# Performance work log

Measured on AMD Instinct MI355X. Metric: run time of the kernel, lower is better.

## Reference

```python
import jax, jax.numpy as jnp
import numpy as np

N_HEADS = 4


def setup_inputs() -> dict:
    key = jax.random.key(0)
    k1, k2, k3 = jax.random.split(key, 3)
    B, C, H, W = 16, 512, 32, 32
    x = jax.random.normal(k1, (B, C, H, W), dtype=jnp.float32)
    # Linear weights stored as (in, out) so y = x @ w + b
    w_proj = jax.random.normal(k2, (C, 3 * C), dtype=jnp.float32) * (C ** -0.5)
    b_proj = jnp.zeros((3 * C,), dtype=jnp.float32)
    w_out = jax.random.normal(k3, (C, C), dtype=jnp.float32) * (C ** -0.5)
    b_out = jnp.zeros((C,), dtype=jnp.float32)
    return {"x": x, "w_proj": w_proj, "b_proj": b_proj, "w_out": w_out, "b_out": b_out}


def reference(x, w_proj, b_proj, w_out, b_out):
    B, C, H, W = x.shape
    d_k = C // N_HEADS
    scale = d_k ** -0.5
    # NOTE: original module defines GroupNorm but never applies it in forward.
    xf = x.reshape(B, C, H * W).transpose(0, 2, 1)          # (B, N, C)
    qkv = xf @ w_proj + b_proj                                # (B, N, 3C)
    qkv = qkv.reshape(B, -1, N_HEADS, 3 * d_k)
    q, k, v = jnp.split(qkv, 3, axis=-1)                      # each (B, N, H, d_k)
    attn = jnp.einsum('bihd,bjhd->bijh', q, k) * scale        # (B, N, N, H)
    attn = jax.nn.softmax(attn, axis=2)                       # softmax over j
    res = jnp.einsum('bijh,bjhd->bihd', attn, v)              # (B, N, H, d_k)
    res = res.reshape(B, -1, N_HEADS * d_k)                   # (B, N, C)
    res = res @ w_out + b_out + xf                            # residual add
    return res.transpose(0, 2, 1).reshape(B, C, H, W)
```

## Files before the change

### kernel.cpp

```cpp
#include <hip/hip_runtime.h>

#define B_  16
#define C_  512
#define N_  1024
#define NH  4
#define DK  128
#define M3  1536

typedef unsigned short u16;
typedef unsigned int   u32;
typedef __attribute__((ext_vector_type(8))) short bfrag;
typedef __attribute__((ext_vector_type(4))) float f4;

#define MFMA(a, b, c) __builtin_amdgcn_mfma_f32_16x16x32_bf16(a, b, c, 0, 0, 0)

#define GL2LDS(gp, lp) __builtin_amdgcn_global_load_lds( \
    (__attribute__((address_space(1))) const unsigned int*)(const void*)(gp), \
    (__attribute__((address_space(3))) unsigned int*)(void*)(lp), 16, 0, 0)

__device__ __forceinline__ u16 f2bf(float f) {
    u32 u = __float_as_uint(f);
    return (u16)((u + 0x7FFFu + ((u >> 16) & 1u)) >> 16);
}
__device__ __forceinline__ float bf2f(u16 h) { return __uint_as_float(((u32)h) << 16); }

#define QSCL 0.12751741859316937f

__global__ __launch_bounds__(256) void conv_split_t(
    const float* __restrict__ src, u16* __restrict__ dhi, u16* __restrict__ dlo,
    int R, int Cc)
{
    __shared__ float Ts[64][65];
    const int tid = threadIdx.x;
    const int c0 = blockIdx.x * 64, r0 = blockIdx.y * 64;
    const size_t bofs = (size_t)blockIdx.z * R * Cc;

#pragma unroll
    for (int p = 0; p < 4; ++p) {
        int r = p * 16 + (tid >> 4);
        int c = (tid & 15) * 4;
        float4 v = *(const float4*)(src + bofs + (size_t)(r0 + r) * Cc + c0 + c);
        Ts[c + 0][r] = v.x; Ts[c + 1][r] = v.y; Ts[c + 2][r] = v.z; Ts[c + 3][r] = v.w;
    }
    __syncthreads();
#pragma unroll
    for (int p = 0; p < 4; ++p) {
        int cc = p * 16 + (tid >> 4);
        int rr = (tid & 15) * 4;
        float f0 = Ts[cc][rr + 0], f1 = Ts[cc][rr + 1];
        float f2 = Ts[cc][rr + 2], f3 = Ts[cc][rr + 3];
        u16 h0 = f2bf(f0), h1 = f2bf(f1), h2 = f2bf(f2), h3 = f2bf(f3);
        u16 l0 = f2bf(f0 - bf2f(h0)), l1 = f2bf(f1 - bf2f(h1));
        u16 l2 = f2bf(f2 - bf2f(h2)), l3 = f2bf(f3 - bf2f(h3));
        size_t o = bofs + (size_t)(c0 + cc) * R + r0 + rr;
        *(uint2*)(void*)(dhi + o) = make_uint2((u32)h0 | ((u32)h1 << 16), (u32)h2 | ((u32)h3 << 16));
        *(uint2*)(void*)(dlo + o) = make_uint2((u32)l0 | ((u32)l1 << 16), (u32)l2 | ((u32)l3 << 16));
    }
}

__global__ __launch_bounds__(256, 2) void qkv_mfma(
    const u16* __restrict__ xt_hi, const u16* __restrict__ xt_lo,
    const u16* __restrict__ wpT_hi, const u16* __restrict__ wpT_lo,
    const float* __restrict__ bp,
    u16* __restrict__ Qh, u16* __restrict__ Ql,
    u16* __restrict__ Kh, u16* __restrict__ Kl,
    u16* __restrict__ Vth, u16* __restrict__ Vtl)
{
    __shared__ __align__(16) u32 SMEM[16512];
    u16* AH = (u16*)SMEM;
    u16* AL = AH + 128 * 64;
    u16* BH = AL + 128 * 64;
    u16* BL = BH + 128 * 64;
    float* FB = (float*)SMEM;

    const int tid = threadIdx.x;
    const int l = tid & 63, w = tid >> 6;
    const int wr = w >> 1, wc = w & 1;
    const int lm = l & 15, kg = l >> 4;
    const int bx = blockIdx.x, by = blockIdx.y, b = blockIdx.z;
    const int m0 = bx * 128, n0 = by * 128;

    const u16* gsrc =
        (w == 0) ? xt_hi + ((size_t)b * N_ + n0) * C_ :
        (w == 1) ? xt_lo + ((size_t)b * N_ + n0) * C_ :
        (w == 2) ? wpT_hi + (size_t)m0 * C_ :
                   wpT_lo + (size_t)m0 * C_;
    u16* ldst = (w == 0) ? AH : (w == 1) ? AL : (w == 2) ? BH : BL;
    const int lane_off = (l >> 3) * C_ + (((l & 7) ^ (l >> 3)) << 3);

    f4 acc[4][4] = {};

    for (int it = 0; it < 8; ++it) {
        __syncthreads();
        const u16* g = gsrc + it * 64 + lane_off;
#pragma unroll
        for (int u = 0; u < 16; ++u)
            GL2LDS(g + (size_t)u * 8 * C_, ldst + u * 512);
        __syncthreads();

#pragma unroll
        for (int kk = 0; kk < 2; ++kk) {
            bfrag ah[4], al[4], bh[4], bl[4];
            const int s = ((kk * 4 + kg) ^ (lm & 7)) << 3;
#pragma unroll
            for (int f = 0; f < 4; ++f) {
                const int ar = wr * 64 + f * 16 + lm;
                const int br = wc * 64 + f * 16 + lm;
                ah[f] = *(const bfrag*)(AH + ar * 64 + s);
                al[f] = *(const bfrag*)(AL + ar * 64 + s);
                bh[f] = *(const bfrag*)(BH + br * 64 + s);
                bl[f] = *(const bfrag*)(BL + br * 64 + s);
            }
#pragma unroll
            for (int i = 0; i < 4; ++i)
#pragma unroll
                for (int j = 0; j < 4; ++j) {
                    acc[i][j] = MFMA(ah[i], bh[j], acc[i][j]);
                    acc[i][j] = MFMA(ah[i], bl[j], acc[i][j]);
                    acc[i][j] = MFMA(al[i], bh[j], acc[i][j]);
                }
        }
    }

    const int hh = bx / 3, t = bx - hh * 3;
    __syncthreads();
    {
        float bias_j[4];
#pragma unroll
        for (int j = 0; j < 4; ++j) bias_j[j] = bp[m0 + wc * 64 + j * 16 + lm];
#pragma unroll
        for (int j = 0; j < 4; ++j) {
            const int col = wc * 64 + j * 16 + lm;
#pragma unroll
            for (int i = 0; i < 4; ++i) {
#pragma unroll
                for (int r = 0; r < 4; ++r) {
                    const int tok = wr * 64 + i * 16 + kg * 4 + r;
                    float v = acc[i][j][r] + bias_j[j];
                    if (t == 0) v *= QSCL;
                    if (t == 2) FB[col * 129 + tok] = v;
                    else        FB[tok * 129 + col] = v;
                }
            }
        }
    }
    __syncthreads();
    {
        const int r2 = tid >> 1, h = tid & 1;
        const float* src = FB + r2 * 129 + h * 64;
        u16* dsth; u16* dstl; size_t o;
        if (t == 2) {
            dsth = Vth; dstl = Vtl;
            o = ((size_t)(b * NH + hh) * DK + r2) * N_ + n0 + h * 64;
        } else {
            dsth = (t == 0) ? Qh : Kh;
            dstl = (t == 0) ? Ql : Kl;
            o = ((size_t)(b * NH + hh) * N_ + n0 + r2) * DK + h * 64;
        }
#pragma unroll
        for (int c0 = 0; c0 < 64; c0 += 8) {
            u16 hb[8], lb[8];
#pragma unroll
            for (int c = 0; c < 8; ++c) {
                float v = src[c0 + c];
                hb[c] = f2bf(v);
                lb[c] = f2bf(v - bf2f(hb[c]));
            }
            *(uint4*)(void*)(dsth + o + c0) = make_uint4(
                (u32)hb[0] | ((u32)hb[1] << 16), (u32)hb[2] | ((u32)hb[3] << 16),
                (u32)hb[4] | ((u32)hb[5] << 16), (u32)hb[6] | ((u32)hb[7] << 16));
            *(uint4*)(void*)(dstl + o + c0) = make_uint4(
                (u32)lb[0] | ((u32)lb[1] << 16), (u32)lb[2] | ((u32)lb[3] << 16),
                (u32)lb[4] | ((u32)lb[5] << 16), (u32)lb[6] | ((u32)lb[7] << 16));
        }
    }
}

__global__ __launch_bounds__(256, 2) void attn_mfma(
    const u16* __restrict__ Qh_, const u16* __restrict__ Ql_,
    const u16* __restrict__ Kh_, const u16* __restrict__ Kl_,
    const u16* __restrict__ Vth_, const u16* __restrict__ Vtl_,
    u16* __restrict__ res_hi, u16* __restrict__ res_lo)
{
    __shared__ __align__(16) u16 KH[32 * 128], KL[32 * 128];
    __shared__ __align__(16) u16 VH[128 * 32], VL[128 * 32];
    __shared__ u16 Ph[4][2][16][40], Pl[4][2][16][40];

    const int tid = threadIdx.x;
    const int l = tid & 63, w = tid >> 6;
    const int lm = l & 15, kg = l >> 4;
    const int bh = blockIdx.x;
    const int qc = blockIdx.y;
    const int i0s = qc * 128 + w * 16 + lm;
    const size_t head = (size_t)bh * N_ * DK;

    bfrag qfh[2][4], qfl[2][4];
#pragma unroll
    for (int s = 0; s < 2; ++s) {
        const u16* qp  = Qh_ + head + (size_t)(i0s + s * 64) * DK + kg * 8;
        const u16* qp2 = Ql_ + head + (size_t)(i0s + s * 64) * DK + kg * 8;
#pragma unroll
        for (int kc = 0; kc < 4; ++kc) {
            qfh[s][kc] = *(const bfrag*)(qp + kc * 32);
            qfl[s][kc] = *(const bfrag*)(qp2 + kc * 32);
        }
    }

    f4 acc_o[2][8] = {};
    float m_r[2] = {-3.0e38f, -3.0e38f}, l_r[2] = {0.f, 0.f};

    for (int jt = 0; jt < 32; ++jt) {
        __syncthreads();
        if (w < 2) {
            const u16* sg = (w & 1) ? Kl_ : Kh_;
            u16* sd = (w & 1) ? KL : KH;
#pragma unroll
            for (int u = 0; u < 8; ++u) {
                const int rbase = u * 4;
                const int row = rbase + (l >> 4);
                GL2LDS(sg + head + (size_t)(jt * 32 + row) * DK + (((l & 15) ^ (row & 7)) << 3),
                       sd + rbase * 128);
            }
        } else {
            const u16* sg = (w & 1) ? Vtl_ : Vth_;
            u16* sd = (w & 1) ? VL : VH;
#pragma unroll
            for (int u = 0; u < 8; ++u) {
                const int rbase = u * 16;
                const int row = rbase + (l >> 2);
                GL2LDS(sg + (size_t)bh * DK * N_ + (size_t)row * N_ + jt * 32
                           + (((l & 3) ^ (row & 3)) << 3),
                       sd + rbase * 32);
            }
        }
        __syncthreads();

        f4 sacc[2][2] = {};
#pragma unroll
        for (int kc = 0; kc < 4; ++kc) {
#pragma unroll
            for (int jf = 0; jf < 2; ++jf) {
                const int row = jf * 16 + lm;
                const int sw = (((kc << 2) | kg) ^ (lm & 7)) << 3;
                bfrag kh = *(const bfrag*)(KH + row * 128 + sw);
                bfrag kl = *(const bfrag*)(KL + row * 128 + sw);
#pragma unroll
                for (int s = 0; s < 2; ++s) {
                    sacc[s][jf] = MFMA(kh, qfh[s][kc], sacc[s][jf]);
                    sacc[s][jf] = MFMA(kh, qfl[s][kc], sacc[s][jf]);
                    sacc[s][jf] = MFMA(kl, qfh[s][kc], sacc[s][jf]);
                }
            }
        }

        float mt[2], mn[2], alpha[2], rs[2];
#pragma unroll
        for (int s = 0; s < 2; ++s) {
            float a = fmaxf(fmaxf(sacc[s][0][0], sacc[s][0][1]),
                            fmaxf(sacc[s][0][2], sacc[s][0][3]));
            float bb = fmaxf(fmaxf(sacc[s][1][0], sacc[s][1][1]),
                             fmaxf(sacc[s][1][2], sacc[s][1][3]));
            mt[s] = fmaxf(a, bb);
        }
        mt[0] = fmaxf(mt[0], __shfl_xor(mt[0], 16));
        mt[1] = fmaxf(mt[1], __shfl_xor(mt[1], 16));
        mt[0] = fmaxf(mt[0], __shfl_xor(mt[0], 32));
        mt[1] = fmaxf(mt[1], __shfl_xor(mt[1], 32));
#pragma unroll
        for (int s = 0; s < 2; ++s) {
            mn[s] = fmaxf(m_r[s], mt[s]);
            alpha[s] = exp2f(m_r[s] - mn[s]);
            m_r[s] = mn[s];
            rs[s] = 0.f;
#pragma unroll
            for (int jf = 0; jf < 2; ++jf) {
                u16 hb[4], lb[4];
#pragma unroll
                for (int r = 0; r < 4; ++r) {
                    float pv = exp2f(sacc[s][jf][r] - mn[s]);
                    rs[s] += pv;
                    hb[r] = f2bf(pv);
                    lb[r] = f2bf(pv - bf2f(hb[r]));
                }
                *(uint2*)(void*)&Ph[w][s][lm][jf * 16 + kg * 4] =
                    make_uint2((u32)hb[0] | ((u32)hb[1] << 16), (u32)hb[2] | ((u32)hb[3] << 16));
                *(uint2*)(void*)&Pl[w][s][lm][jf * 16 + kg * 4] =
                    make_uint2((u32)lb[0] | ((u32)lb[1] << 16), (u32)lb[2] | ((u32)lb[3] << 16));
            }
        }
        rs[0] += __shfl_xor(rs[0], 16);
        rs[1] += __shfl_xor(rs[1], 16);
        rs[0] += __shfl_xor(rs[0], 32);
        rs[1] += __shfl_xor(rs[1], 32);
#pragma unroll
        for (int s = 0; s < 2; ++s) {
            l_r[s] = l_r[s] * alpha[s] + rs[s];
#pragma unroll
            for (int df = 0; df < 8; ++df)
#pragma unroll
                for (int r = 0; r < 4; ++r) acc_o[s][df][r] *= alpha[s];
        }

        bfrag pbh0 = *(const bfrag*)&Ph[w][0][lm][kg * 8];
        bfrag pbl0 = *(const bfrag*)&Pl[w][0][lm][kg * 8];
        bfrag pbh1 = *(const bfrag*)&Ph[w][1][lm][kg * 8];
        bfrag pbl1 = *(const bfrag*)&Pl[w][1][lm][kg * 8];
#pragma unroll
        for (int df = 0; df < 8; ++df) {
            const int row = df * 16 + lm;
            const int sw = (kg ^ (lm & 3)) << 3;
            bfrag vh = *(const bfrag*)(VH + row * 32 + sw);
            bfrag vl = *(const bfrag*)(VL + row * 32 + sw);
            acc_o[0][df] = MFMA(vh, pbh0, acc_o[0][df]);
            acc_o[0][df] = MFMA(vh, pbl0, acc_o[0][df]);
            acc_o[0][df] = MFMA(vl, pbh0, acc_o[0][df]);
            acc_o[1][df] = MFMA(vh, pbh1, acc_o[1][df]);
            acc_o[1][df] = MFMA(vh, pbl1, acc_o[1][df]);
            acc_o[1][df] = MFMA(vl, pbh1, acc_o[1][df]);
        }
    }

    const int b = bh >> 2, h = bh & 3;
#pragma unroll
    for (int s = 0; s < 2; ++s) {
        const float inv = 1.f / l_r[s];
        const size_t ro = ((size_t)b * N_ + i0s + s * 64) * C_ + h * DK;
#pragma unroll
        for (int df = 0; df < 8; ++df) {
            u16 hb[4], lb[4];
#pragma unroll
            for (int r = 0; r < 4; ++r) {
                float v = acc_o[s][df][r] * inv;
                hb[r] = f2bf(v);
                lb[r] = f2bf(v - bf2f(hb[r]));
            }
            const size_t o = ro + df * 16 + kg * 4;
            *(uint2*)(void*)(res_hi + o) = make_uint2((u32)hb[0] | ((u32)hb[1] << 16),
                                                      (u32)hb[2] | ((u32)hb[3] << 16));
            *(uint2*)(void*)(res_lo + o) = make_uint2((u32)lb[0] | ((u32)lb[1] << 16),
                                                      (u32)lb[2] | ((u32)lb[3] << 16));
        }
    }
}

__global__ __launch_bounds__(256, 2) void out_mfma(
    const u16* __restrict__ woT_hi, const u16* __restrict__ woT_lo,
    const u16* __restrict__ res_hi, const u16* __restrict__ res_lo,
    const float* __restrict__ bo, const float* __restrict__ x,
    float* __restrict__ out)
{
    __shared__ __align__(16) u16 AH[128 * 64], AL[128 * 64], BH[128 * 64], BL[128 * 64];
    const int tid = threadIdx.x;
    const int l = tid & 63, w = tid >> 6;
    const int wr = w >> 1, wc = w & 1;
    const int lm = l & 15, kg = l >> 4;
    const int bx = blockIdx.x, by = blockIdx.y, b = blockIdx.z;
    const int c0 = bx * 128, n0 = by * 128;

    const u16* gsrc =
        (w == 0) ? woT_hi + (size_t)c0 * C_ :
        (w == 1) ? woT_lo + (size_t)c0 * C_ :
        (w == 2) ? res_hi + ((size_t)b * N_ + n0) * C_ :
                   res_lo + ((size_t)b * N_ + n0) * C_;
    u16* ldst = (w == 0) ? AH : (w == 1) ? AL : (w == 2) ? BH : BL;
    const int lane_off = (l >> 3) * C_ + (((l & 7) ^ (l >> 3)) << 3);

    f4 acc[4][4] = {};

    for (int it = 0; it < 8; ++it) {
        __syncthreads();
        const u16* g = gsrc + it * 64 + lane_off;
#pragma unroll
        for (int u = 0; u < 16; ++u)
            GL2LDS(g + (size_t)u * 8 * C_, ldst + u * 512);
        __syncthreads();

#pragma unroll
        for (int kk = 0; kk < 2; ++kk) {
            bfrag ah[4], al[4], bh[4], bl[4];
            const int s = ((kk * 4 + kg) ^ (lm & 7)) << 3;
#pragma unroll
            for (int f = 0; f < 4; ++f) {
                const int ar = wr * 64 + f * 16 + lm;
                const int br = wc * 64 + f * 16 + lm;
                ah[f] = *(const bfrag*)(AH + ar * 64 + s);
                al[f] = *(const bfrag*)(AL + ar * 64 + s);
                bh[f] = *(const bfrag*)(BH + br * 64 + s);
                bl[f] = *(const bfrag*)(BL + br * 64 + s);
            }
#pragma unroll
            for (int i = 0; i < 4; ++i)
#pragma unroll
                for (int j = 0; j < 4; ++j) {
                    acc[i][j] = MFMA(ah[i], bh[j], acc[i][j]);
                    acc[i][j] = MFMA(ah[i], bl[j], acc[i][j]);
                    acc[i][j] = MFMA(al[i], bh[j], acc[i][j]);
                }
        }
    }

#pragma unroll
    for (int j = 0; j < 4; ++j) {
        const int ncol = n0 + wc * 64 + j * 16 + lm;
#pragma unroll
        for (int i = 0; i < 4; ++i) {
#pragma unroll
            for (int r = 0; r < 4; ++r) {
                const int crow = c0 + wr * 64 + i * 16 + kg * 4 + r;
                const size_t o = ((size_t)b * C_ + crow) * N_ + ncol;
                out[o] = acc[i][j][r] + bo[crow] + x[o];
            }
        }
    }
}

extern "C" void kernel_launch(void* const* d_in, const int* in_sizes, int n_in,
                              void* d_out, int out_size, void* d_ws, size_t ws_size,
                              hipStream_t stream) {
    const float* x  = (const float*)d_in[0];
    const float* wp = (const float*)d_in[1];
    const float* bp = (const float*)d_in[2];
    const float* wo = (const float*)d_in[3];
    const float* bo = (const float*)d_in[4];
    float* out = (float*)d_out;

    const size_t SEG = (size_t)B_ * N_ * C_;
    u16* xt_hi = (u16*)d_ws;
    u16* xt_lo = xt_hi + SEG;
    u16* Qh  = xt_hi + 2 * SEG;
    u16* Ql  = Qh + SEG;
    u16* Kh  = Ql + SEG;
    u16* Kl  = Kh + SEG;
    u16* Vth = Kl + SEG;
    u16* Vtl = Vth + SEG;
    u16* res_hi = xt_hi;
    u16* res_lo = xt_lo;
    u16* woT_hi = Qh;
    u16* woT_lo = woT_hi + C_ * C_;
    u16* wpT_hi = (u16*)d_out;
    u16* wpT_lo = wpT_hi + C_ * M3;

    conv_split_t<<<dim3(16, 8, 16), 256, 0, stream>>>(x, xt_hi, xt_lo, C_, N_);
    conv_split_t<<<dim3(24, 8, 1), 256, 0, stream>>>(wp, wpT_hi, wpT_lo, C_, M3);
    qkv_mfma<<<dim3(12, 8, 16), 256, 0, stream>>>(xt_hi, xt_lo, wpT_hi, wpT_lo, bp,
                                                  Qh, Ql, Kh, Kl, Vth, Vtl);
    attn_mfma<<<dim3(64, 8), 256, 0, stream>>>(Qh, Ql, Kh, Kl, Vth, Vtl, res_hi, res_lo);
    conv_split_t<<<dim3(8, 8, 1), 256, 0, stream>>>(wo, woT_hi, woT_lo, C_, C_);
    out_mfma<<<dim3(4, 8, 16), 256, 0, stream>>>(woT_hi, woT_lo, res_hi, res_lo, bo, x, out);
}
```

Before: 373.9 us.

## Store QKV directly from registers, skip unneeded rescale, raise MFMA priority

The QKV GEMM epilogue now writes bf16 hi/lo results straight from accumulator registers instead of staging them through an LDS transpose buffer. This removes two barriers and the LDS round trip, but Q/K get scattered 2-byte stores. The attention kernel skips the output rescale when the wave-wide running max did not change, and uses truncation instead of rounding for the P hi part. It also wraps the MFMA sections in s_setprio so matrix work gets scheduling priority over other waves.

```diff
diff --git a/kernel.cpp b/kernel.cpp
--- a/kernel.cpp
+++ b/kernel.cpp
@@ -66,13 +66,7 @@
     u16* __restrict__ Kh, u16* __restrict__ Kl,
     u16* __restrict__ Vth, u16* __restrict__ Vtl)
 {
-    __shared__ __align__(16) u32 SMEM[16512];
-    u16* AH = (u16*)SMEM;
-    u16* AL = AH + 128 * 64;
-    u16* BH = AL + 128 * 64;
-    u16* BL = BH + 128 * 64;
-    float* FB = (float*)SMEM;
-
+    __shared__ __align__(16) u16 AH[128 * 64], AL[128 * 64], BH[128 * 64], BL[128 * 64];
     const int tid = threadIdx.x;
     const int l = tid & 63, w = tid >> 6;
     const int wr = w >> 1, wc = w & 1;
@@ -123,55 +117,40 @@
     }
 
     const int hh = bx / 3, t = bx - hh * 3;
-    __syncthreads();
-    {
-        float bias_j[4];
-#pragma unroll
-        for (int j = 0; j < 4; ++j) bias_j[j] = bp[m0 + wc * 64 + j * 16 + lm];
-#pragma unroll
-        for (int j = 0; j < 4; ++j) {
-            const int col = wc * 64 + j * 16 + lm;
-#pragma unroll
-            for (int i = 0; i < 4; ++i) {
+#pragma unroll
+    for (int j = 0; j < 4; ++j) {
+        const int mcol = m0 + wc * 64 + j * 16 + lm;
+        const float bias = bp[mcol];
+        const int d = mcol & 127;
+#pragma unroll
+        for (int i = 0; i < 4; ++i) {
+            const int tok = n0 + wr * 64 + i * 16 + kg * 4;
+            if (t == 2) {
+                u16 hb[4], lb[4];
 #pragma unroll
                 for (int r = 0; r < 4; ++r) {
-                    const int tok = wr * 64 + i * 16 + kg * 4 + r;
-                    float v = acc[i][j][r] + bias_j[j];
+                    float v = acc[i][j][r] + bias;
+                    hb[r] = f2bf(v);
+                    lb[r] = f2bf(v - bf2f(hb[r]));
+                }
+                const size_t o = ((size_t)(b * NH + hh) * DK + d) * N_ + tok;
+                *(uint2*)(void*)(Vth + o) = make_uint2((u32)hb[0] | ((u32)hb[1] << 16),
+                                                       (u32)hb[2] | ((u32)hb[3] << 16));
+                *(uint2*)(void*)(Vtl + o) = make_uint2((u32)lb[0] | ((u32)lb[1] << 16),
+                                                       (u32)lb[2] | ((u32)lb[3] << 16));
+            } else {
+                u16* dh = (t == 0) ? Qh : Kh;
+                u16* dl = (t == 0) ? Ql : Kl;
+                const size_t o = ((size_t)(b * NH + hh) * N_ + tok) * DK + d;
+#pragma unroll
+                for (int r = 0; r < 4; ++r) {
+                    float v = acc[i][j][r] + bias;
                     if (t == 0) v *= QSCL;
-                    if (t == 2) FB[col * 129 + tok] = v;
-                    else        FB[tok * 129 + col] = v;
-                }
-            }
-        }
-    }
-    __syncthreads();
-    {
-        const int r2 = tid >> 1, h = tid & 1;
-        const float* src = FB + r2 * 129 + h * 64;
-        u16* dsth; u16* dstl; size_t o;
-        if (t == 2) {
-            dsth = Vth; dstl = Vtl;
-            o = ((size_t)(b * NH + hh) * DK + r2) * N_ + n0 + h * 64;
-        } else {
-            dsth = (t == 0) ? Qh : Kh;
-            dstl = (t == 0) ? Ql : Kl;
-            o = ((size_t)(b * NH + hh) * N_ + n0 + r2) * DK + h * 64;
-        }
-#pragma unroll
-        for (int c0 = 0; c0 < 64; c0 += 8) {
-            u16 hb[8], lb[8];
-#pragma unroll
-            for (int c = 0; c < 8; ++c) {
-                float v = src[c0 + c];
-                hb[c] = f2bf(v);
-                lb[c] = f2bf(v - bf2f(hb[c]));
-            }
-            *(uint4*)(void*)(dsth + o + c0) = make_uint4(
-                (u32)hb[0] | ((u32)hb[1] << 16), (u32)hb[2] | ((u32)hb[3] << 16),
-                (u32)hb[4] | ((u32)hb[5] << 16), (u32)hb[6] | ((u32)hb[7] << 16));
-            *(uint4*)(void*)(dstl + o + c0) = make_uint4(
-                (u32)lb[0] | ((u32)lb[1] << 16), (u32)lb[2] | ((u32)lb[3] << 16),
-                (u32)lb[4] | ((u32)lb[5] << 16), (u32)lb[6] | ((u32)lb[7] << 16));
+                    u16 hb = f2bf(v);
+                    dh[o + (size_t)r * DK] = hb;
+                    dl[o + (size_t)r * DK] = f2bf(v - bf2f(hb));
+                }
+            }
         }
     }
 }
@@ -236,6 +215,7 @@
         __syncthreads();
 
         f4 sacc[2][2] = {};
+        __builtin_amdgcn_s_setprio(1);
 #pragma unroll
         for (int kc = 0; kc < 4; ++kc) {
 #pragma unroll
@@ -252,8 +232,9 @@
                 }
             }
         }
-
-        float mt[2], mn[2], alpha[2], rs[2];
+        __builtin_amdgcn_s_setprio(0);
+
+        float mt[2], rs[2];
 #pragma unroll
         for (int s = 0; s < 2; ++s) {
             float a = fmaxf(fmaxf(sacc[s][0][0], sacc[s][0][1]),
@@ -268,18 +249,25 @@
         mt[1] = fmaxf(mt[1], __shfl_xor(mt[1], 32));
 #pragma unroll
         for (int s = 0; s < 2; ++s) {
-            mn[s] = fmaxf(m_r[s], mt[s]);
-            alpha[s] = exp2f(m_r[s] - mn[s]);
-            m_r[s] = mn[s];
+            const float mn = fmaxf(m_r[s], mt[s]);
+            if (!__all(mt[s] <= m_r[s])) {
+                const float alpha = exp2f(m_r[s] - mn);
+                l_r[s] *= alpha;
+#pragma unroll
+                for (int df = 0; df < 8; ++df)
+#pragma unroll
+                    for (int r = 0; r < 4; ++r) acc_o[s][df][r] *= alpha;
+            }
+            m_r[s] = mn;
             rs[s] = 0.f;
 #pragma unroll
             for (int jf = 0; jf < 2; ++jf) {
                 u16 hb[4], lb[4];
 #pragma unroll
                 for (int r = 0; r < 4; ++r) {
-                    float pv = exp2f(sacc[s][jf][r] - mn[s]);
+                    float pv = exp2f(sacc[s][jf][r] - mn);
                     rs[s] += pv;
-                    hb[r] = f2bf(pv);
+                    hb[r] = (u16)(__float_as_uint(pv) >> 16);
                     lb[r] = f2bf(pv - bf2f(hb[r]));
                 }
                 *(uint2*)(void*)&Ph[w][s][lm][jf * 16 + kg * 4] =
@@ -292,19 +280,14 @@
         rs[1] += __shfl_xor(rs[1], 16);
         rs[0] += __shfl_xor(rs[0], 32);
         rs[1] += __shfl_xor(rs[1], 32);
-#pragma unroll
-        for (int s = 0; s < 2; ++s) {
-            l_r[s] = l_r[s] * alpha[s] + rs[s];
-#pragma unroll
-            for (int df = 0; df < 8; ++df)
-#pragma unroll
-                for (int r = 0; r < 4; ++r) acc_o[s][df][r] *= alpha[s];
-        }
+        l_r[0] += rs[0];
+        l_r[1] += rs[1];
 
         bfrag pbh0 = *(const bfrag*)&Ph[w][0][lm][kg * 8];
         bfrag pbl0 = *(const bfrag*)&Pl[w][0][lm][kg * 8];
         bfrag pbh1 = *(const bfrag*)&Ph[w][1][lm][kg * 8];
         bfrag pbl1 = *(const bfrag*)&Pl[w][1][lm][kg * 8];
+        __builtin_amdgcn_s_setprio(1);
 #pragma unroll
         for (int df = 0; df < 8; ++df) {
             const int row = df * 16 + lm;
@@ -318,6 +301,7 @@
             acc_o[1][df] = MFMA(vh, pbl1, acc_o[1][df]);
             acc_o[1][df] = MFMA(vl, pbh1, acc_o[1][df]);
         }
+        __builtin_amdgcn_s_setprio(0);
     }
 
     const int b = bh >> 2, h = bh & 3;
```

Result: faster. 341.0 us (-8.8%).
